# Kernel tuning notes

Measured on AMD Instinct MI355X. Metric: run time of the kernel, lower is better.

The kernel has to match this reference:

```python
import jax, jax.numpy as jnp
import numpy as np

N_NODES = 50000


def gcn_conv(x, W, b, src, dst, n_nodes):
    """PyG GCNConv: h = D^-1/2 (A + I) D^-1/2 (x W) + b, with self-loops."""
    h = x @ W  # [N, out]
    loop = jnp.arange(n_nodes, dtype=src.dtype)
    s = jnp.concatenate([src, loop])  # [E+N]
    d = jnp.concatenate([dst, loop])
    # degree of destination nodes (self-loops guarantee deg >= 1)
    deg = jax.ops.segment_sum(jnp.ones_like(d, dtype=h.dtype), d, num_segments=n_nodes)
    dinv = jax.lax.rsqrt(deg)  # deg >= 1 so safe
    norm = dinv[s] * dinv[d]  # [E+N]
    msg = h[s] * norm[:, None]  # gather + scale (per-edge messages)
    out = jax.ops.segment_sum(msg, d, num_segments=n_nodes)  # scatter-add
    return out + b


def setup_inputs() -> dict:
    key = jax.random.key(0)
    ks = jax.random.split(key, 8)
    in_d, hid, out_d = 128, 128, 64
    x = jax.random.normal(ks[0], (N_NODES, in_d), dtype=jnp.float32)
    edge_index = jax.random.randint(ks[1], (2, 800000), 0, N_NODES, dtype=jnp.int64)
    def glorot(k, fan_in, fan_out):
        lim = float(np.sqrt(6.0 / (fan_in + fan_out)))
        return jax.random.uniform(k, (fan_in, fan_out), jnp.float32, -lim, lim)
    return {
        "x": x,
        "edge_index": edge_index,
        "W1": glorot(ks[2], in_d, hid),
        "b1": jnp.zeros((hid,), jnp.float32),
        "W2": glorot(ks[3], hid, hid),
        "b2": jnp.zeros((hid,), jnp.float32),
        "W3": glorot(ks[4], hid, out_d),
        "b3": jnp.zeros((out_d,), jnp.float32),
    }


def reference(x, edge_index, W1, b1, W2, b2, W3, b3):
    src, dst = edge_index[0], edge_index[1]
    n = x.shape[0]
    h = jax.nn.relu(gcn_conv(x, W1, b1, src, dst, n))
    h = jax.nn.relu(gcn_conv(h, W2, b2, src, dst, n))
    return gcn_conv(h, W3, b3, src, dst, n)
```

## Files before the change

### kernel.cpp

```cpp
#include <hip/hip_runtime.h>
#include <stdint.h>
#include <stddef.h>

#define EE 800000
#define CAP 64

typedef __attribute__((ext_vector_type(8))) short bf16x8;
typedef __attribute__((ext_vector_type(4))) float f32x4;

__device__ __forceinline__ float bflo(uint32_t p) { return __uint_as_float(p << 16); }
__device__ __forceinline__ float bfhi(uint32_t p) { return __uint_as_float(p & 0xffff0000u); }
__device__ __forceinline__ float bf1(unsigned short u) { return __uint_as_float(((uint32_t)u) << 16); }
__device__ __forceinline__ unsigned short f2bf(float v) {
  uint32_t b = __float_as_uint(v);
  b += 0x7fffu + ((b >> 16) & 1u);
  return (unsigned short)(b >> 16);
}

__device__ __forceinline__ void wt_work(int idx, const float* W1, const float* W2,
                                        const float* W3, unsigned short* Wt1,
                                        unsigned short* Wt2, unsigned short* Wt3) {
  if (idx < 16384) {
    int k = idx >> 7, n = idx & 127;
    Wt1[n * 128 + k] = f2bf(W1[idx]);
  } else if (idx < 32768) {
    int l = idx - 16384, k = l >> 7, n = l & 127;
    Wt2[n * 128 + k] = f2bf(W2[l]);
  } else if (idx < 40960) {
    int l = idx - 32768, k = l >> 6, n = l & 63;
    Wt3[n * 128 + k] = f2bf(W3[l]);
  }
}

__global__ void k12_fillslot(const int* ei, int* cnt, int* slots, int E, int N,
                             int* viol, const float* W1, const float* W2,
                             const float* W3, unsigned short* Wt1,
                             unsigned short* Wt2, unsigned short* Wt3) {
  int nfb = (E + 255) / 256;
  if ((int)blockIdx.x >= nfb) {
    wt_work((blockIdx.x - nfb) * 256 + threadIdx.x, W1, W2, W3, Wt1, Wt2, Wt3);
    return;
  }
  bool is64 = ((ei[1] | ei[3] | ei[5] | ei[7] | ei[9] | ei[11] | ei[13] | ei[15]) == 0);
  int e = blockIdx.x * 256 + threadIdx.x;
  if (e >= E) return;
  int s, d;
  if (is64) {
    const uint2* e64 = (const uint2*)ei;
    s = (int)e64[e].x;
    d = (int)e64[(size_t)E + e].x;
  } else {
    s = ei[e];
    d = ei[(size_t)E + e];
  }
  if ((unsigned)s >= (unsigned)N || (unsigned)d >= (unsigned)N) {
    atomicOr(viol, 1);
    return;
  }
  int pos = atomicAdd(&cnt[d], 1);
  if (pos < CAP) slots[(size_t)d * CAP + pos] = s;
}

__global__ void k12_dinv(const int* cnt, float* dinv, int N, int* viol) {
  int i = blockIdx.x * 256 + threadIdx.x;
  if (i >= N) return;
  int c = cnt[i];
  if (c > CAP) atomicOr(viol, 2);
  dinv[i] = rsqrtf((float)(c + 1));
}

__global__ __launch_bounds__(256) void k12_wt(const float* W1, const float* W2,
                                              const float* W3, unsigned short* Wt1,
                                              unsigned short* Wt2, unsigned short* Wt3) {
  wt_work(blockIdx.x * 256 + threadIdx.x, W1, W2, W3, Wt1, Wt2, Wt3);
}

__global__ void k12_hist(const int* ei, int* cnt, int E, int N, int* viol) {
  bool is64 = ((ei[1] | ei[3] | ei[5] | ei[7] | ei[9] | ei[11] | ei[13] | ei[15]) == 0);
  if (blockIdx.x == 0 && threadIdx.x == 0) viol[1] = is64 ? 1 : 0;
  int e = blockIdx.x * 256 + threadIdx.x;
  if (e >= E) return;
  int s, d;
  if (is64) {
    const uint2* e64 = (const uint2*)ei;
    s = (int)e64[e].x;
    d = (int)e64[(size_t)E + e].x;
  } else {
    s = ei[e];
    d = ei[(size_t)E + e];
  }
  if ((unsigned)s >= (unsigned)N || (unsigned)d >= (unsigned)N) {
    atomicOr(viol, 1);
    return;
  }
  atomicAdd(&cnt[d], 1);
}

__global__ __launch_bounds__(256) void k12_scanA(const int* cnt, int* partial, int N) {
  __shared__ int sc[256];
  int t = threadIdx.x;
  int n = blockIdx.x * 256 + t;
  sc[t] = (n < N) ? cnt[n] : 0;
  __syncthreads();
  for (int s = 128; s > 0; s >>= 1) {
    if (t < s) sc[t] += sc[t + s];
    __syncthreads();
  }
  if (t == 0) partial[blockIdx.x] = sc[0];
}

__global__ __launch_bounds__(256) void k12_scanB(int* partial, int* off, int nsb,
                                                 int N, int E, int* viol) {
  __shared__ int sc[256];
  int t = threadIdx.x;
  int v = (t < nsb) ? partial[t] : 0;
  sc[t] = v;
  __syncthreads();
  for (int d = 1; d < 256; d <<= 1) {
    int w = (t >= d) ? sc[t - d] : 0;
    __syncthreads();
    sc[t] += w;
    __syncthreads();
  }
  if (t < nsb) partial[t] = sc[t] - v;
  if (t == 255) {
    off[N] = sc[255];
    if (sc[255] != E) atomicOr(viol, 4);
  }
}

__global__ __launch_bounds__(256) void k12_scanC(const int* cnt, const int* partial,
                                                 int* off, int* cur, float* dinv, int N) {
  __shared__ int sc[256];
  int t = threadIdx.x;
  int n = blockIdx.x * 256 + t;
  int v = (n < N) ? cnt[n] : 0;
  sc[t] = v;
  __syncthreads();
  for (int d = 1; d < 256; d <<= 1) {
    int w = (t >= d) ? sc[t - d] : 0;
    __syncthreads();
    sc[t] += w;
    __syncthreads();
  }
  if (n < N) {
    int o = partial[blockIdx.x] + sc[t] - v;
    off[n] = o;
    cur[n] = o;
    dinv[n] = rsqrtf((float)(v + 1));
  }
}

__global__ void k12_fillcsr(const int* ei, int* cur, int* adj, int E, int N,
                            const int* viol) {
  int is64 = viol[1];
  int e = blockIdx.x * 256 + threadIdx.x;
  if (e >= E) return;
  int s, d;
  if (is64) {
    const uint2* e64 = (const uint2*)ei;
    s = (int)e64[e].x;
    d = (int)e64[(size_t)E + e].x;
  } else {
    s = ei[e];
    d = ei[(size_t)E + e];
  }
  if ((unsigned)s >= (unsigned)N || (unsigned)d >= (unsigned)N) return;
  int pos = atomicAdd(&cur[d], 1);
  adj[pos] = s;
}

__global__ __launch_bounds__(256) void k12_gemmX(const float* __restrict__ X,
                                                 const unsigned short* __restrict__ Wt,
                                                 unsigned short* __restrict__ OUT,
                                                 int M) {
  const int tid = threadIdx.x;
  const int wid = tid >> 6, lane = tid & 63;
  const int quad = lane >> 4, r16 = lane & 15;
  const int m0 = blockIdx.x * 64 + wid * 16;
  const int mrow = m0 + r16;

  f32x4 acc[8];
#pragma unroll
  for (int ct = 0; ct < 8; ++ct) acc[ct] = {0.f, 0.f, 0.f, 0.f};

#pragma unroll
  for (int kk = 0; kk < 4; ++kk) {
    bf16x8 a = {0, 0, 0, 0, 0, 0, 0, 0};
    if (mrow < M) {
      const float* xp = X + (size_t)mrow * 128 + kk * 32 + quad * 8;
      float4 u0 = *(const float4*)xp;
      float4 u1 = *(const float4*)(xp + 4);
      a[0] = (short)f2bf(u0.x); a[1] = (short)f2bf(u0.y);
      a[2] = (short)f2bf(u0.z); a[3] = (short)f2bf(u0.w);
      a[4] = (short)f2bf(u1.x); a[5] = (short)f2bf(u1.y);
      a[6] = (short)f2bf(u1.z); a[7] = (short)f2bf(u1.w);
    }
#pragma unroll
    for (int ct = 0; ct < 8; ++ct) {
      bf16x8 b = *(const bf16x8*)(Wt + (size_t)(ct * 16 + r16) * 128 + kk * 32 + quad * 8);
      acc[ct] = __builtin_amdgcn_mfma_f32_16x16x32_bf16(a, b, acc[ct], 0, 0, 0);
    }
  }
#pragma unroll
  for (int ct = 0; ct < 8; ++ct) {
    int col = ct * 16 + r16;
#pragma unroll
    for (int r = 0; r < 4; ++r) {
      int row = m0 + quad * 4 + r;
      if (row < M) OUT[(size_t)row * 128 + col] = f2bf(acc[ct][r]);
    }
  }
}

template <int F>
__global__ __launch_bounds__(256) void k12_gemmB(const unsigned short* __restrict__ X,
                                                 const unsigned short* __restrict__ Wt,
                                                 unsigned short* __restrict__ OUT,
                                                 int M) {
  const int tid = threadIdx.x;
  const int wid = tid >> 6, lane = tid & 63;
  const int quad = lane >> 4, r16 = lane & 15;
  const int m0 = blockIdx.x * 64 + wid * 16;
  const int mrow = m0 + r16;
  constexpr int CT = F / 16;

  f32x4 acc[CT];
#pragma unroll
  for (int ct = 0; ct < CT; ++ct) acc[ct] = {0.f, 0.f, 0.f, 0.f};

#pragma unroll
  for (int kk = 0; kk < 4; ++kk) {
    bf16x8 a = {0, 0, 0, 0, 0, 0, 0, 0};
    if (mrow < M) a = *(const bf16x8*)(X + (size_t)mrow * 128 + kk * 32 + quad * 8);
#pragma unroll
    for (int ct = 0; ct < CT; ++ct) {
      bf16x8 b = *(const bf16x8*)(Wt + (size_t)(ct * 16 + r16) * 128 + kk * 32 + quad * 8);
      acc[ct] = __builtin_amdgcn_mfma_f32_16x16x32_bf16(a, b, acc[ct], 0, 0, 0);
    }
  }
#pragma unroll
  for (int ct = 0; ct < CT; ++ct) {
    int col = ct * 16 + r16;
#pragma unroll
    for (int r = 0; r < 4; ++r) {
      int row = m0 + quad * 4 + r;
      if (row < M) OUT[(size_t)row * F + col] = f2bf(acc[ct][r]);
    }
  }
}

template <int SLOT>
__global__ __launch_bounds__(256) void k12_agg128(const unsigned short* __restrict__ t,
                                                  const int* __restrict__ cntoff,
                                                  const int* __restrict__ adj,
                                                  const float* __restrict__ dinv,
                                                  const float* __restrict__ bias,
                                                  unsigned short* __restrict__ out,
                                                  int N) {
  int i = (blockIdx.x * 256 + threadIdx.x) >> 6;
  int lane = threadIdx.x & 63;
  if (i >= N) return;
  const uint32_t* hb = (const uint32_t*)t;
  float di = dinv[i];
  int j0, deg;
  if (SLOT) {
    j0 = i * CAP;
    deg = cntoff[i];
    if (deg > CAP) deg = CAP;
  } else {
    j0 = cntoff[i];
    deg = cntoff[i + 1] - j0;
  }

  uint32_t ps = hb[(size_t)i * 64 + lane];
  float ax = di * bflo(ps), ay = di * bfhi(ps);

  for (int jb = 0; jb < deg; jb += 64) {
    int nb = deg - jb;
    if (nb > 64) nb = 64;
    int myj = jb + lane;
    int sj = 0;
    float wj = 0.f;
    if (myj < deg) {
      sj = adj[j0 + myj];
      wj = dinv[sj];
    }
    int j = 0;
    for (; j + 8 <= nb; j += 8) {
      int s0 = __shfl(sj, j + 0), s1 = __shfl(sj, j + 1);
      int s2 = __shfl(sj, j + 2), s3 = __shfl(sj, j + 3);
      int s4 = __shfl(sj, j + 4), s5 = __shfl(sj, j + 5);
      int s6 = __shfl(sj, j + 6), s7 = __shfl(sj, j + 7);
      float w0 = __shfl(wj, j + 0), w1 = __shfl(wj, j + 1);
      float w2 = __shfl(wj, j + 2), w3 = __shfl(wj, j + 3);
      float w4 = __shfl(wj, j + 4), w5 = __shfl(wj, j + 5);
      float w6 = __shfl(wj, j + 6), w7 = __shfl(wj, j + 7);
      uint32_t p0 = hb[(size_t)s0 * 64 + lane];
      uint32_t p1 = hb[(size_t)s1 * 64 + lane];
      uint32_t p2 = hb[(size_t)s2 * 64 + lane];
      uint32_t p3 = hb[(size_t)s3 * 64 + lane];
      uint32_t p4 = hb[(size_t)s4 * 64 + lane];
      uint32_t p5 = hb[(size_t)s5 * 64 + lane];
      uint32_t p6 = hb[(size_t)s6 * 64 + lane];
      uint32_t p7 = hb[(size_t)s7 * 64 + lane];
      ax = fmaf(w0, bflo(p0), ax); ay = fmaf(w0, bfhi(p0), ay);
      ax = fmaf(w1, bflo(p1), ax); ay = fmaf(w1, bfhi(p1), ay);
      ax = fmaf(w2, bflo(p2), ax); ay = fmaf(w2, bfhi(p2), ay);
      ax = fmaf(w3, bflo(p3), ax); ay = fmaf(w3, bfhi(p3), ay);
      ax = fmaf(w4, bflo(p4), ax); ay = fmaf(w4, bfhi(p4), ay);
      ax = fmaf(w5, bflo(p5), ax); ay = fmaf(w5, bfhi(p5), ay);
      ax = fmaf(w6, bflo(p6), ax); ay = fmaf(w6, bfhi(p6), ay);
      ax = fmaf(w7, bflo(p7), ax); ay = fmaf(w7, bfhi(p7), ay);
    }
    for (; j + 2 <= nb; j += 2) {
      int s0 = __shfl(sj, j + 0), s1 = __shfl(sj, j + 1);
      float w0 = __shfl(wj, j + 0), w1 = __shfl(wj, j + 1);
      uint32_t p0 = hb[(size_t)s0 * 64 + lane];
      uint32_t p1 = hb[(size_t)s1 * 64 + lane];
      ax = fmaf(w0, bflo(p0), ax); ay = fmaf(w0, bfhi(p0), ay);
      ax = fmaf(w1, bflo(p1), ax); ay = fmaf(w1, bfhi(p1), ay);
    }
    if (j < nb) {
      int s = __shfl(sj, j);
      float w = __shfl(wj, j);
      uint32_t p = hb[(size_t)s * 64 + lane];
      ax = fmaf(w, bflo(p), ax); ay = fmaf(w, bfhi(p), ay);
    }
  }
  float2 bp = ((const float2*)bias)[lane];
  ax = fmaxf(fmaf(ax, di, bp.x), 0.f);
  ay = fmaxf(fmaf(ay, di, bp.y), 0.f);
  ((uint32_t*)out)[(size_t)i * 64 + lane] =
      (uint32_t)f2bf(ax) | ((uint32_t)f2bf(ay) << 16);
}

template <int SLOT>
__global__ __launch_bounds__(256) void k12_agg64(const unsigned short* __restrict__ t,
                                                 const int* __restrict__ cntoff,
                                                 const int* __restrict__ adj,
                                                 const float* __restrict__ dinv,
                                                 const float* __restrict__ bias,
                                                 float* __restrict__ out, int N) {
  int i = (blockIdx.x * 256 + threadIdx.x) >> 6;
  int lane = threadIdx.x & 63;
  if (i >= N) return;
  float di = dinv[i];
  int j0, deg;
  if (SLOT) {
    j0 = i * CAP;
    deg = cntoff[i];
    if (deg > CAP) deg = CAP;
  } else {
    j0 = cntoff[i];
    deg = cntoff[i + 1] - j0;
  }

  float a = di * bf1(t[(size_t)i * 64 + lane]);

  for (int jb = 0; jb < deg; jb += 64) {
    int nb = deg - jb;
    if (nb > 64) nb = 64;
    int myj = jb + lane;
    int sj = 0;
    float wj = 0.f;
    if (myj < deg) {
      sj = adj[j0 + myj];
      wj = dinv[sj];
    }
    int j = 0;
    for (; j + 8 <= nb; j += 8) {
      int s0 = __shfl(sj, j + 0), s1 = __shfl(sj, j + 1);
      int s2 = __shfl(sj, j + 2), s3 = __shfl(sj, j + 3);
      int s4 = __shfl(sj, j + 4), s5 = __shfl(sj, j + 5);
      int s6 = __shfl(sj, j + 6), s7 = __shfl(sj, j + 7);
      float w0 = __shfl(wj, j + 0), w1 = __shfl(wj, j + 1);
      float w2 = __shfl(wj, j + 2), w3 = __shfl(wj, j + 3);
      float w4 = __shfl(wj, j + 4), w5 = __shfl(wj, j + 5);
      float w6 = __shfl(wj, j + 6), w7 = __shfl(wj, j + 7);
      float p0 = bf1(t[(size_t)s0 * 64 + lane]);
      float p1 = bf1(t[(size_t)s1 * 64 + lane]);
      float p2 = bf1(t[(size_t)s2 * 64 + lane]);
      float p3 = bf1(t[(size_t)s3 * 64 + lane]);
      float p4 = bf1(t[(size_t)s4 * 64 + lane]);
      float p5 = bf1(t[(size_t)s5 * 64 + lane]);
      float p6 = bf1(t[(size_t)s6 * 64 + lane]);
      float p7 = bf1(t[(size_t)s7 * 64 + lane]);
      a = fmaf(w0, p0, a); a = fmaf(w1, p1, a);
      a = fmaf(w2, p2, a); a = fmaf(w3, p3, a);
      a = fmaf(w4, p4, a); a = fmaf(w5, p5, a);
      a = fmaf(w6, p6, a); a = fmaf(w7, p7, a);
    }
    for (; j < nb; ++j) {
      int s = __shfl(sj, j);
      float w = __shfl(wj, j);
      a = fmaf(w, bf1(t[(size_t)s * 64 + lane]), a);
    }
  }
  out[(size_t)i * 64 + lane] = fmaf(a, di, bias[lane]);
}

__global__ void k12_sent(const int* viol, float* out, int hc4, int hc7) {
  if (threadIdx.x != 0 || blockIdx.x != 0) return;
  int v = viol[0];
  if (v & 1) out[1] = 1200.f;
  if (v & 2) out[6] = 2200.f;
  if (v & 4) out[2] = 1300.f;
  if (hc4)   out[4] = 1800.f;
  if (hc7)   out[7] = 2400.f;
}

__global__ void k12_wsrep(float* out, float code) {
  if (threadIdx.x == 0 && blockIdx.x == 0) out[3] = code;
}

extern "C" void kernel_launch(void* const* d_in, const int* in_sizes, int n_in,
                              void* d_out, int out_size, void* d_ws, size_t ws_size,
                              hipStream_t stream) {
  if (n_in < 8) {
    hipMemsetAsync(d_out, 0, (size_t)out_size * 4, stream);
    k12_wsrep<<<1, 64, 0, stream>>>((float*)d_out, 2500.f + n_in);
    return;
  }
  const float* x  = (const float*)d_in[0];
  const int* ei   = (const int*)d_in[1];
  const float* W1 = (const float*)d_in[2];
  const float* b1 = (const float*)d_in[3];
  const float* W2 = (const float*)d_in[4];
  const float* b2 = (const float*)d_in[5];
  const float* W3 = (const float*)d_in[6];
  const float* b3 = (const float*)d_in[7];

  const int N = in_sizes[0] / 128;
  int hc7 = (N == 50000) ? 0 : 1;
  int E = in_sizes[1] / 2;
  int hc4 = 0;
  if (in_sizes[1] == 2 * EE || in_sizes[1] == 4 * EE) E = EE;
  else hc4 = 1;

  char* base = (char*)d_ws;
  size_t o = 0;
  auto carve = [&](size_t bytes) {
    char* q = base + o;
    o += (bytes + 255) & ~(size_t)255;
    return q;
  };
  int* viol   = (int*)carve(256);
  int* cnt    = (int*)carve((size_t)N * 4);
  float* dinv = (float*)carve((size_t)N * 4);
  unsigned short* Wt1 = (unsigned short*)carve(16384 * 2);
  unsigned short* Wt2 = (unsigned short*)carve(16384 * 2);
  unsigned short* Wt3 = (unsigned short*)carve(8192 * 2);
  unsigned short* T   = (unsigned short*)carve((size_t)N * 128 * 2);
  unsigned short* B   = (unsigned short*)carve((size_t)N * 128 * 2);
  size_t common = o;

  int* slots = (int*)carve((size_t)N * CAP * 4);
  size_t slot_need = o;
  o = common;
  int* off     = (int*)carve((size_t)(N + 1) * 4);
  int* cur     = (int*)carve((size_t)N * 4);
  int* partial = (int*)carve(256 * 4);
  int* adj     = (int*)carve((size_t)E * 4);
  size_t csr_need = o;

  bool use_slot = (ws_size >= slot_need);
  if (!use_slot && ws_size < csr_need) {
    hipMemsetAsync(d_out, 0, (size_t)out_size * 4, stream);
    int wsmb = (int)(ws_size >> 20);
    if (wsmb > 20000) wsmb = 20000;
    k12_wsrep<<<1, 64, 0, stream>>>((float*)d_out, 4000.f + (float)wsmb);
    return;
  }

  hipMemsetAsync(cnt, 0, (size_t)N * 4, stream);
  hipMemsetAsync(viol, 0, 16, stream);

  const int ablocks = (N + 3) / 4;
  const int gblocks = (N + 63) / 64;
  const int nfb = (E + 255) / 256;

  if (use_slot) {
    k12_fillslot<<<nfb + 160, 256, 0, stream>>>(ei, cnt, slots, E, N, viol, W1, W2,
                                                W3, Wt1, Wt2, Wt3);
    k12_dinv<<<(N + 255) / 256, 256, 0, stream>>>(cnt, dinv, N, viol);

    k12_gemmX<<<gblocks, 256, 0, stream>>>(x, Wt1, T, N);
    k12_agg128<1><<<ablocks, 256, 0, stream>>>(T, cnt, slots, dinv, b1, B, N);
    k12_gemmB<128><<<gblocks, 256, 0, stream>>>(B, Wt2, T, N);
    k12_agg128<1><<<ablocks, 256, 0, stream>>>(T, cnt, slots, dinv, b2, B, N);
    k12_gemmB<64><<<gblocks, 256, 0, stream>>>(B, Wt3, T, N);
    k12_agg64<1><<<ablocks, 256, 0, stream>>>(T, cnt, slots, dinv, b3,
                                              (float*)d_out, N);
  } else {
    const int nsb = (N + 255) / 256;
    k12_wt<<<160, 256, 0, stream>>>(W1, W2, W3, Wt1, Wt2, Wt3);
    k12_hist<<<nfb, 256, 0, stream>>>(ei, cnt, E, N, viol);
    k12_scanA<<<nsb, 256, 0, stream>>>(cnt, partial, N);
    k12_scanB<<<1, 256, 0, stream>>>(partial, off, nsb, N, E, viol);
    k12_scanC<<<nsb, 256, 0, stream>>>(cnt, partial, off, cur, dinv, N);
    k12_fillcsr<<<nfb, 256, 0, stream>>>(ei, cur, adj, E, N, viol);

    k12_gemmX<<<gblocks, 256, 0, stream>>>(x, Wt1, T, N);
    k12_agg128<0><<<ablocks, 256, 0, stream>>>(T, off, adj, dinv, b1, B, N);
    k12_gemmB<128><<<gblocks, 256, 0, stream>>>(B, Wt2, T, N);
    k12_agg128<0><<<ablocks, 256, 0, stream>>>(T, off, adj, dinv, b2, B, N);
    k12_gemmB<64><<<gblocks, 256, 0, stream>>>(B, Wt3, T, N);
    k12_agg64<0><<<ablocks, 256, 0, stream>>>(T, off, adj, dinv, b3,
                                              (float*)d_out, N);
  }
  k12_sent<<<1, 64, 0, stream>>>(viol, (float*)d_out, hc4, hc7);
}
```

Measured before the change: 289.9 us.

## Partition slot-fill by destination range across 8 block groups for atomic locality

The edge-to-slot fill kernel now splits destination nodes into 8 ranges, each handled by its own group of 256 blocks. Every group scans all edges through a grid-stride loop but only does atomics and slot writes for destinations in its range. The intent is to keep the cnt atomics and slot writes within a smaller working set that fits better in L2 per XCD, and the index loads are marked nontemporal. The cost is that the destination indices are read 8 times.

```diff
diff --git a/kernel.cpp b/kernel.cpp
--- a/kernel.cpp
+++ b/kernel.cpp
@@ -4,6 +4,7 @@
 
 #define EE 800000
 #define CAP 64
+#define FB_G 256
 
 typedef __attribute__((ext_vector_type(8))) short bf16x8;
 typedef __attribute__((ext_vector_type(4))) float f32x4;
@@ -32,33 +33,46 @@
   }
 }
 
-__global__ void k12_fillslot(const int* ei, int* cnt, int* slots, int E, int N,
+__global__ void k13_fillslot(const int* ei, int* cnt, int* slots, int E, int N,
                              int* viol, const float* W1, const float* W2,
                              const float* W3, unsigned short* Wt1,
                              unsigned short* Wt2, unsigned short* Wt3) {
-  int nfb = (E + 255) / 256;
-  if ((int)blockIdx.x >= nfb) {
-    wt_work((blockIdx.x - nfb) * 256 + threadIdx.x, W1, W2, W3, Wt1, Wt2, Wt3);
+  if ((int)blockIdx.x >= 8 * FB_G) {
+    wt_work(((int)blockIdx.x - 8 * FB_G) * 256 + threadIdx.x, W1, W2, W3, Wt1,
+            Wt2, Wt3);
     return;
   }
-  bool is64 = ((ei[1] | ei[3] | ei[5] | ei[7] | ei[9] | ei[11] | ei[13] | ei[15]) == 0);
-  int e = blockIdx.x * 256 + threadIdx.x;
-  if (e >= E) return;
-  int s, d;
-  if (is64) {
-    const uint2* e64 = (const uint2*)ei;
-    s = (int)e64[e].x;
-    d = (int)e64[(size_t)E + e].x;
-  } else {
-    s = ei[e];
-    d = ei[(size_t)E + e];
-  }
-  if ((unsigned)s >= (unsigned)N || (unsigned)d >= (unsigned)N) {
-    atomicOr(viol, 1);
-    return;
-  }
-  int pos = atomicAdd(&cnt[d], 1);
-  if (pos < CAP) slots[(size_t)d * CAP + pos] = s;
+  const int p = (int)blockIdx.x & 7;
+  const int cb = (int)blockIdx.x >> 3;
+  const int lo = (int)(((long long)N * p) >> 3);
+  const int hi = (int)(((long long)N * (p + 1)) >> 3);
+  const bool is64 =
+      ((ei[1] | ei[3] | ei[5] | ei[7] | ei[9] | ei[11] | ei[13] | ei[15]) == 0);
+
+  for (int e0 = cb * 256; e0 < E; e0 += FB_G * 256) {
+    int e = e0 + (int)threadIdx.x;
+    if (e >= E) break;
+    int d;
+    if (is64) {
+      d = __builtin_nontemporal_load((const int*)ei + 2 * ((size_t)E + e));
+    } else {
+      d = __builtin_nontemporal_load(ei + (size_t)E + e);
+    }
+    if (p == 0 && (unsigned)d >= (unsigned)N) atomicOr(viol, 1);
+    if (d < lo || d >= hi) continue;
+    int s;
+    if (is64) {
+      s = __builtin_nontemporal_load((const int*)ei + 2 * (size_t)e);
+    } else {
+      s = __builtin_nontemporal_load(ei + e);
+    }
+    if ((unsigned)s >= (unsigned)N) {
+      atomicOr(viol, 1);
+      continue;
+    }
+    int pos = atomicAdd(&cnt[d], 1);
+    if (pos < CAP) slots[(size_t)d * CAP + pos] = s;
+  }
 }
 
 __global__ void k12_dinv(const int* cnt, float* dinv, int N, int* viol) {
@@ -481,8 +495,8 @@
   const int nfb = (E + 255) / 256;
 
   if (use_slot) {
-    k12_fillslot<<<nfb + 160, 256, 0, stream>>>(ei, cnt, slots, E, N, viol, W1, W2,
-                                                W3, Wt1, Wt2, Wt3);
+    k13_fillslot<<<8 * FB_G + 160, 256, 0, stream>>>(ei, cnt, slots, E, N, viol,
+                                                     W1, W2, W3, Wt1, Wt2, Wt3);
     k12_dinv<<<(N + 255) / 256, 256, 0, stream>>>(cnt, dinv, N, viol);
 
     k12_gemmX<<<gblocks, 256, 0, stream>>>(x, Wt1, T, N);
```

Result: faster. 277.6 us (-4.2%).
